# Performance work log

Hardware: AMD Instinct MI355X
Metric: run time of the kernel (lower is better)

## Reference

```python
import jax, jax.numpy as jnp
import numpy as np

N = 5000      # nodes per event (hardcoded in PFNet7.forward)
BIN = 100     # LSH bin_size
K = 16        # kNN per node within bin
SLOPE = 0.01  # LeakyReLU default negative slope


def _mlp(x, W1, b1, W2, b2, W3, b3):
    h = jax.nn.leaky_relu(x @ W1 + b1, SLOPE)
    h = jax.nn.leaky_relu(h @ W2 + b2, SLOPE)
    return h @ W3 + b3


def _build_graph_lsh(x, codebook):
    # x: [N, F]. Faithful vectorized version of GraphBuildingLSH (batch=1).
    n_bins = N // BIN                                   # 50
    mul = x @ codebook[:, : n_bins // 2]                # [N, 25]
    cmul = jnp.concatenate([mul, -mul], axis=-1)        # [N, 50]
    bin_idx = jnp.argmax(cmul, axis=-1)                 # [N]
    bins_split = jnp.argsort(bin_idx).reshape(n_bins, BIN)  # [nb, BIN]
    pts = x[bins_split]                                 # [nb, BIN, F]
    dm = jax.nn.sigmoid(jnp.einsum('pif,pjf->pij', pts, pts))  # [nb, BIN, BIN]
    vals, inds = jax.lax.top_k(dm, K)                   # [nb, BIN, K]
    src = jnp.broadcast_to(bins_split[:, :, None], inds.shape).reshape(-1)
    dst = jnp.take_along_axis(bins_split, inds.reshape(n_bins, -1), axis=1).reshape(-1)
    val = vals.reshape(-1)                              # [nb*BIN*K] = 80000 edges
    return src, dst, val


def _gcn_conv(x, W, b, src, dst, ew):
    # PyG GCNConv: add self-loops (weight 1), symmetric normalization, aggregate at col.
    n = x.shape[0]
    loop = jnp.arange(n)
    row = jnp.concatenate([src, loop])
    col = jnp.concatenate([dst, loop])
    w = jnp.concatenate([ew, jnp.ones((n,), x.dtype)])
    deg = jax.ops.segment_sum(w, col, num_segments=n)
    dis = jnp.where(deg > 0, deg ** -0.5, 0.0)
    norm = dis[row] * w * dis[col]
    h = x @ W
    out = jax.ops.segment_sum(norm[:, None] * h[row], col, num_segments=n)
    return out + b


def _graph_conv(x, Wrel, brel, Wroot, src, dst, ew):
    # PyG GraphConv(aggr='add'): lin_rel(sum_j w_ij x_j) + lin_root(x)
    agg = jax.ops.segment_sum(ew[:, None] * x[src], dst, num_segments=x.shape[0])
    return agg @ Wrel + brel + x @ Wroot


def setup_inputs() -> dict:
    key = jax.random.key(0)
    ks = jax.random.split(key, 24)
    f32 = jnp.float32
    d = {
        'x': jax.random.normal(ks[0], (N, 12), f32),
        'ygen_id': jax.random.normal(ks[1], (N, 6), f32),
        'ygen': jax.random.normal(ks[2], (N, 6), f32),
        'codebook': jax.random.normal(ks[3], (12, 100), f32),
        # nn1: 12 -> 125 -> 125 -> 12
        'nn1_W1': jax.random.normal(ks[4], (12, 125), f32) * 0.1,
        'nn1_b1': jnp.zeros((125,), f32),
        'nn1_W2': jax.random.normal(ks[5], (125, 125), f32) * 0.1,
        'nn1_b2': jnp.zeros((125,), f32),
        'nn1_W3': jax.random.normal(ks[6], (125, 12), f32) * 0.1,
        'nn1_b3': jnp.zeros((12,), f32),
        # GCNConv: 12 -> 32
        'gcn_W': jax.random.normal(ks[7], (12, 32), f32) * 0.1,
        'gcn_b': jnp.zeros((32,), f32),
        # GraphConv: 32 -> 32
        'gc_Wrel': jax.random.normal(ks[8], (32, 32), f32) * 0.1,
        'gc_brel': jnp.zeros((32,), f32),
        'gc_Wroot': jax.random.normal(ks[9], (32, 32), f32) * 0.1,
        # nn2: 32 -> 125 -> 125 -> 6
        'nn2_W1': jax.random.normal(ks[10], (32, 125), f32) * 0.1,
        'nn2_b1': jnp.zeros((125,), f32),
        'nn2_W2': jax.random.normal(ks[11], (125, 125), f32) * 0.1,
        'nn2_b2': jnp.zeros((125,), f32),
        'nn2_W3': jax.random.normal(ks[12], (125, 6), f32) * 0.1,
        'nn2_b3': jnp.zeros((6,), f32),
        # nn3: 38 -> 125 -> 125 -> 6
        'nn3_W1': jax.random.normal(ks[13], (38, 125), f32) * 0.1,
        'nn3_b1': jnp.zeros((125,), f32),
        'nn3_W2': jax.random.normal(ks[14], (125, 125), f32) * 0.1,
        'nn3_b2': jnp.zeros((125,), f32),
        'nn3_W3': jax.random.normal(ks[15], (125, 6), f32) * 0.1,
        'nn3_b3': jnp.zeros((6,), f32),
    }
    return d


def reference(x, ygen_id, ygen, codebook,
              nn1_W1, nn1_b1, nn1_W2, nn1_b2, nn1_W3, nn1_b3,
              gcn_W, gcn_b, gc_Wrel, gc_brel, gc_Wroot,
              nn2_W1, nn2_b1, nn2_W2, nn2_b2, nn2_W3, nn2_b3,
              nn3_W1, nn3_b1, nn3_W2, nn3_b2, nn3_W3, nn3_b3):
    h = _mlp(x, nn1_W1, nn1_b1, nn1_W2, nn1_b2, nn1_W3, nn1_b3)   # [N, 12]
    src, dst, ew = _build_graph_lsh(h, codebook)
    h = jax.nn.leaky_relu(h, SLOPE)
    h = _gcn_conv(h, gcn_W, gcn_b, src, dst, ew)                   # [N, 32]
    h = _graph_conv(h, gc_Wrel, gc_brel, gc_Wroot, src, dst, ew)
    h = jax.nn.leaky_relu(h, SLOPE)
    cand_ids = _mlp(h, nn2_W1, nn2_b1, nn2_W2, nn2_b2, nn2_W3, nn2_b3)
    cand_p4 = _mlp(jnp.concatenate([h, cand_ids], axis=-1),
                   nn3_W1, nn3_b1, nn3_W2, nn3_b2, nn3_W3, nn3_b3)
    return (cand_ids, cand_p4, ygen_id, ygen)
```

## Files before the change

kernel.cpp:

```cpp
#include <hip/hip_runtime.h>
#include <math.h>

#define NN 5000
#define NBINS 50
#define BINSZ 100
#define KNN 16
#define BPAD 104
#define MROWS 112
#define NB 20

typedef _Float16 half8 __attribute__((ext_vector_type(8)));

__device__ __forceinline__ float lrelu(float x){ return x >= 0.f ? x : 0.01f*x; }

__global__ __launch_bounds__(640) void nn1_kernel(
    const float* __restrict__ x,
    const float* __restrict__ W1, const float* __restrict__ b1,
    const float* __restrict__ W2, const float* __restrict__ b2,
    const float* __restrict__ W3, const float* __restrict__ b3,
    const float* __restrict__ cb,
    float* __restrict__ h_out, int* __restrict__ bin_idx) {
    __shared__ float sW[8000];
    __shared__ float bufX[12 * NB];
    __shared__ float bufA[125 * NB];
    __shared__ float bufB[125 * NB];
    __shared__ float sCB[300];
    int tid = threadIdx.x;
    int n0 = blockIdx.x * NB;
    int g = tid >> 7, j = tid & 127;
    float acc[4];
    float4 r0, r1; float rt = 0.f;

    if (tid < 60) {
        float4 v = ((const float4*)(x + n0 * 12))[tid];
        int e = tid * 4;
        bufX[(e % 12) * NB + (e / 12)] = v.x;
        bufX[((e + 1) % 12) * NB + ((e + 1) / 12)] = v.y;
        bufX[((e + 2) % 12) * NB + ((e + 2) / 12)] = v.z;
        bufX[((e + 3) % 12) * NB + ((e + 3) / 12)] = v.w;
    }
    if (tid < 300) { int k = tid / 25, c = tid - k * 25; sCB[tid] = cb[k * 100 + c]; }
    if (tid < 375) ((float4*)sW)[tid] = ((const float4*)W1)[tid];
    __syncthreads();

    if (j < 125) {
        float bj = b1[j];
        acc[0] = bj; acc[1] = bj; acc[2] = bj; acc[3] = bj;
        #pragma unroll
        for (int k = 0; k < 12; ++k) {
            float w = sW[k * 125 + j];
            float4 a = *(const float4*)&bufX[k * NB + g * 4];
            acc[0] += a.x * w; acc[1] += a.y * w; acc[2] += a.z * w; acc[3] += a.w * w;
        }
        #pragma unroll
        for (int n = 0; n < 4; ++n) bufA[j * NB + g * 4 + n] = lrelu(acc[n]);
    }
    r0 = (tid < 1000) ? ((const float4*)W2)[tid] : make_float4(0.f,0.f,0.f,0.f);
    r1 = (tid < 360)  ? ((const float4*)W2)[tid + 640] : make_float4(0.f,0.f,0.f,0.f);
    __syncthreads();
    if (tid < 1000) ((float4*)sW)[tid] = r0;
    if (tid < 360)  ((float4*)sW)[tid + 640] = r1;
    __syncthreads();

    if (j < 125) { float bj = b2[j]; acc[0] = bj; acc[1] = bj; acc[2] = bj; acc[3] = bj; }
    for (int c = 0; c < 4; ++c) {
        if (c < 3) {
            int base = (c + 1) * 1000, nf4 = (c + 1 < 3) ? 1000 : 906;
            r0 = (tid < nf4) ? ((const float4*)W2)[base + tid] : make_float4(0.f,0.f,0.f,0.f);
            r1 = (tid + 640 < nf4) ? ((const float4*)W2)[base + tid + 640] : make_float4(0.f,0.f,0.f,0.f);
            if (c + 1 == 3 && tid == 0) rt = W2[15624];
        }
        int nk = (c < 3) ? 32 : 29;
        const float* wbuf = sW + (c & 1) * 4000;
        if (j < 125) {
            const float* arow = &bufA[(c * 32) * NB + g * 4];
            for (int k = 0; k < nk; ++k) {
                float w = wbuf[k * 125 + j];
                float4 a = *(const float4*)&arow[k * NB];
                acc[0] += a.x * w; acc[1] += a.y * w; acc[2] += a.z * w; acc[3] += a.w * w;
            }
        }
        if (c < 3) {
            float* dst = sW + ((c + 1) & 1) * 4000;
            int nf4 = (c + 1 < 3) ? 1000 : 906;
            if (tid < nf4) ((float4*)dst)[tid] = r0;
            if (tid + 640 < nf4) ((float4*)dst)[tid + 640] = r1;
            if (c + 1 == 3 && tid == 0) dst[3624] = rt;
            __syncthreads();
        }
    }
    if (j < 125) {
        #pragma unroll
        for (int n = 0; n < 4; ++n) bufB[j * NB + g * 4 + n] = lrelu(acc[n]);
    }
    __syncthreads();
    if (tid < 375) ((float4*)sW)[tid] = ((const float4*)W3)[tid];
    __syncthreads();

    if (j < 48) {
        int jj = j % 12, s = j / 12;
        int k0 = s * 32, nk = (s < 3) ? 32 : 29;
        float ps[4] = {0.f, 0.f, 0.f, 0.f};
        for (int k = 0; k < nk; ++k) {
            float w = sW[(k0 + k) * 12 + jj];
            float4 a = *(const float4*)&bufB[(k0 + k) * NB + g * 4];
            ps[0] += a.x * w; ps[1] += a.y * w; ps[2] += a.z * w; ps[3] += a.w * w;
        }
        #pragma unroll
        for (int n = 0; n < 4; ++n) bufA[(s * 12 + jj) * NB + g * 4 + n] = ps[n];
    }
    __syncthreads();
    if (tid < 240) {
        int jj = tid / 20, n = tid % 20;
        float v = bufA[jj * NB + n] + bufA[(12 + jj) * NB + n]
                + bufA[(24 + jj) * NB + n] + bufA[(36 + jj) * NB + n] + b3[jj];
        h_out[(n0 + n) * 12 + jj] = v;
        bufB[jj * NB + n] = v;
    }
    __syncthreads();

    if (tid < NB) {
        int n = tid;
        float hv[12];
        #pragma unroll
        for (int k = 0; k < 12; ++k) hv[k] = bufB[k * NB + n];
        float best = -INFINITY; int bi = 0;
        for (int c = 0; c < 25; ++c) {
            float m = 0.f;
            #pragma unroll
            for (int k = 0; k < 12; ++k) m += hv[k] * sCB[k * 25 + c];
            if (m > best) { best = m; bi = c; }
        }
        for (int c = 0; c < 25; ++c) {
            float m = 0.f;
            #pragma unroll
            for (int k = 0; k < 12; ++k) m += hv[k] * sCB[k * 25 + c];
            if (-m > best) { best = -m; bi = c + 25; }
        }
        bin_idx[n0 + n] = bi;
    }
}

__global__ __launch_bounds__(64) void scatter_kernel(
    const int* __restrict__ bin_idx, int* __restrict__ order) {
    __shared__ int sBI[NN];
    int b = blockIdx.x, lane = threadIdx.x;
    for (int t = lane; t < NN / 4; t += 64) ((int4*)sBI)[t] = ((const int4*)bin_idx)[t];
    __syncthreads();
    unsigned long long below = (lane == 0) ? 0ULL : ((~0ULL) >> (64 - lane));
    int cnt_lt = 0;
    for (int base = 0; base < NN; base += 64) {
        int i = base + lane;
        int bi = (i < NN) ? sBI[i] : 999;
        cnt_lt += __popcll(__ballot(bi < b));
    }
    int offs = cnt_lt;
    for (int base = 0; base < NN; base += 64) {
        int i = base + lane;
        int bi = (i < NN) ? sBI[i] : 999;
        unsigned long long m = __ballot(bi == b);
        if (bi == b) order[offs + __popcll(m & below)] = i;
        offs += __popcll(m);
    }
}

__global__ __launch_bounds__(256) void build_kernel(
    const float* __restrict__ h, const int* __restrict__ order,
    _Float16* __restrict__ Mg, float* __restrict__ dis_g) {
    __shared__ _Float16 M[BINSZ * BPAD];
    __shared__ float s_h[BINSZ * 12];
    __shared__ int   s_nodes[BINSZ];
    __shared__ unsigned s_tv[200 * KNN];
    int p = blockIdx.x, tid = threadIdx.x;

    if (tid < BINSZ) s_nodes[tid] = order[p * BINSZ + tid];
    for (int t = tid; t < BINSZ * BPAD / 2; t += 256) ((int*)M)[t] = 0;
    __syncthreads();
    for (int t = tid; t < BINSZ * 12; t += 256) {
        int i = t / 12, k = t - i * 12;
        s_h[t] = h[s_nodes[i] * 12 + k];
    }
    __syncthreads();

    if (tid < 200) {
        int row = tid >> 1, half = tid & 1;
        const float4* xp = (const float4*)&s_h[row * 12];
        float4 x0 = xp[0], x1 = xp[1], x2 = xp[2];
        unsigned tv[KNN];
        #pragma unroll
        for (int k = 0; k < KNN; ++k) tv[k] = 0u;
        int j0 = half * 50;
        for (int jj = 0; jj < 50; ++jj) {
            int j = j0 + jj;
            const float4* ap = (const float4*)&s_h[j * 12];
            float4 a0 = ap[0], a1 = ap[1], a2 = ap[2];
            float d = x0.x*a0.x + x0.y*a0.y + x0.z*a0.z + x0.w*a0.w
                    + x1.x*a1.x + x1.y*a1.y + x1.z*a1.z + x1.w*a1.w
                    + x2.x*a2.x + x2.y*a2.y + x2.z*a2.z + x2.w*a2.w;
            float v = 1.f / (1.f + expf(-d));
            unsigned key = (__float_as_uint(v) & 0xFFFFFF80u) | (unsigned)(127 - j);
            if (key > tv[KNN - 1]) {
                unsigned ins = key;
                #pragma unroll
                for (int k = 0; k < KNN; ++k) {
                    bool gt = ins > tv[k];
                    unsigned mx = gt ? ins : tv[k];
                    unsigned mn = gt ? tv[k] : ins;
                    tv[k] = mx; ins = mn;
                }
            }
        }
        #pragma unroll
        for (int k = 0; k < KNN; ++k) s_tv[tid * KNN + k] = tv[k];
    }
    __syncthreads();

    if (tid < BINSZ) {
        int base = tid * 32;
        int ia = 0, ib = 0;
        #pragma unroll
        for (int k = 0; k < KNN; ++k) {
            unsigned av = s_tv[base + ia], bv = s_tv[base + 16 + ib];
            bool tA = av > bv;
            unsigned key = tA ? av : bv;
            ia += tA; ib += !tA;
            int ix = 127 - (int)(key & 127u);
            float v = __uint_as_float(key & 0xFFFFFF80u);
            M[ix * BPAD + tid] = (_Float16)v;
        }
    }
    __syncthreads();

    for (int t = tid; t < BINSZ * BPAD / 8; t += 256)
        ((uint4*)(Mg + (size_t)p * BINSZ * BPAD))[t] = ((const uint4*)M)[t];
    if (tid < BINSZ) {
        float dsum = 1.0f;
        #pragma unroll 13
        for (int sc = 0; sc < 13; ++sc) {
            half8 m = *(const half8*)&M[tid * BPAD + sc * 8];
            dsum += (float)m[0] + (float)m[1] + (float)m[2] + (float)m[3]
                  + (float)m[4] + (float)m[5] + (float)m[6] + (float)m[7];
        }
        dis_g[p * BINSZ + tid] = 1.0f / sqrtf(dsum);
    }
}

__global__ __launch_bounds__(128) void conv_kernel(
    const _Float16* __restrict__ Mg, const float* __restrict__ dis_g,
    const float* __restrict__ h, const int* __restrict__ order,
    const float* __restrict__ gcn_W, const float* __restrict__ gcn_b,
    float* __restrict__ gcn_n, float* __restrict__ agg_n,
    const float4* __restrict__ ygen_id4, const float4* __restrict__ ygen4,
    float4* __restrict__ out4) {
    __shared__ _Float16 M[MROWS * BPAD];
    __shared__ float s_h[BINSZ * 12];
    __shared__ int   s_nodes[BINSZ];
    __shared__ float s_dis[BINSZ];
    __shared__ float s_w[12 * 8];
    __shared__ float s_hWd[8 * BPAD];
    __shared__ float s_gcn[8 * BPAD];
    int bid = blockIdx.x, tid = threadIdx.x;
    int p = bid >> 2, cg = bid & 3, c0 = cg * 8;

    if (tid < 75) {
        int gI = bid * 75 + tid;
        out4[15000 + gI] = (gI < 7500) ? ygen_id4[gI] : ygen4[gI - 7500];
    }
    if (tid < BINSZ) {
        s_nodes[tid] = order[p * BINSZ + tid];
        s_dis[tid]   = dis_g[p * BINSZ + tid];
    }
    for (int t = tid; t < 96; t += 128)
        s_w[t] = gcn_W[(t >> 3) * 32 + c0 + (t & 7)];
    for (int t = tid; t < BINSZ * BPAD / 8; t += 128)
        ((uint4*)M)[t] = ((const uint4*)(Mg + (size_t)p * BINSZ * BPAD))[t];
    for (int t = tid; t < (MROWS - BINSZ) * BPAD / 2; t += 128)
        ((int*)(M + BINSZ * BPAD))[t] = 0;
    if (tid < 32) {
        s_hWd[(tid >> 2) * BPAD + 100 + (tid & 3)] = 0.f;
        s_gcn[(tid >> 2) * BPAD + 100 + (tid & 3)] = 0.f;
    }
    __syncthreads();
    for (int t = tid; t < BINSZ * 12; t += 128) {
        int i = t / 12, k = t - i * 12;
        s_h[t] = h[s_nodes[i] * 12 + k];
    }
    __syncthreads();

    for (int o = tid; o < BINSZ * 8; o += 128) {
        int s = o >> 3, cc = o & 7;
        float a = 0.f;
        #pragma unroll
        for (int k = 0; k < 12; ++k) a += lrelu(s_h[s * 12 + k]) * s_w[k * 8 + cc];
        s_hWd[cc * BPAD + s] = s_dis[s] * a;
    }
    __syncthreads();

    int cc = tid & 7, dg = tid >> 3;
    {
        float acc[7];
        #pragma unroll
        for (int r = 0; r < 7; ++r) acc[r] = 0.f;
        for (int sc = 0; sc < 13; ++sc) {
            float4 hv0 = *(const float4*)&s_hWd[cc * BPAD + sc * 8];
            float4 hv1 = *(const float4*)&s_hWd[cc * BPAD + sc * 8 + 4];
            #pragma unroll
            for (int r = 0; r < 7; ++r) {
                int d = dg + 16 * r;
                half8 m = *(const half8*)&M[d * BPAD + sc * 8];
                acc[r] += (float)m[0]*hv0.x + (float)m[1]*hv0.y + (float)m[2]*hv0.z + (float)m[3]*hv0.w
                        + (float)m[4]*hv1.x + (float)m[5]*hv1.y + (float)m[6]*hv1.z + (float)m[7]*hv1.w;
            }
        }
        float bc = gcn_b[c0 + cc];
        #pragma unroll
        for (int r = 0; r < 7; ++r) {
            int d = dg + 16 * r;
            if (d < BINSZ) {
                float gq = s_dis[d] * (acc[r] + s_hWd[cc * BPAD + d]) + bc;
                s_gcn[cc * BPAD + d] = gq;
                gcn_n[s_nodes[d] * 32 + c0 + cc] = gq;
            }
        }
    }
    __syncthreads();
    {
        float acc[7];
        #pragma unroll
        for (int r = 0; r < 7; ++r) acc[r] = 0.f;
        for (int sc = 0; sc < 13; ++sc) {
            float4 hv0 = *(const float4*)&s_gcn[cc * BPAD + sc * 8];
            float4 hv1 = *(const float4*)&s_gcn[cc * BPAD + sc * 8 + 4];
            #pragma unroll
            for (int r = 0; r < 7; ++r) {
                int d = dg + 16 * r;
                half8 m = *(const half8*)&M[d * BPAD + sc * 8];
                acc[r] += (float)m[0]*hv0.x + (float)m[1]*hv0.y + (float)m[2]*hv0.z + (float)m[3]*hv0.w
                        + (float)m[4]*hv1.x + (float)m[5]*hv1.y + (float)m[6]*hv1.z + (float)m[7]*hv1.w;
            }
        }
        #pragma unroll
        for (int r = 0; r < 7; ++r) {
            int d = dg + 16 * r;
            if (d < BINSZ) agg_n[s_nodes[d] * 32 + c0 + cc] = acc[r];
        }
    }
}

__global__ __launch_bounds__(640) void nn23_kernel(
    const float* __restrict__ gcn_n, const float* __restrict__ agg_n,
    const float* __restrict__ Wrel, const float* __restrict__ brel,
    const float* __restrict__ Wroot,
    const float* __restrict__ A1, const float* __restrict__ ab1,
    const float* __restrict__ A2, const float* __restrict__ ab2,
    const float* __restrict__ A3, const float* __restrict__ ab3,
    const float* __restrict__ B1, const float* __restrict__ bb1,
    const float* __restrict__ B2, const float* __restrict__ bb2,
    const float* __restrict__ B3, const float* __restrict__ bb3,
    float* __restrict__ out_ids, float* __restrict__ out_p4) {
    __shared__ float sW[8000];
    __shared__ float sAG[32 * NB];
    __shared__ float sGC[32 * NB];
    __shared__ float bufC[38 * NB];
    __shared__ float bufA[125 * NB];
    __shared__ float bufB[125 * NB];
    int tid = threadIdx.x;
    int n0 = blockIdx.x * NB;
    int g = tid >> 7, j = tid & 127;
    float acc[4];
    float4 r0, r1; float rt = 0.f;

    if (tid < 160) {
        float4 va = ((const float4*)(agg_n + n0 * 32))[tid];
        float4 vg = ((const float4*)(gcn_n + n0 * 32))[tid];
        int e = tid * 4, n = e / 32, k = e % 32;
        sAG[k * NB + n] = va.x; sAG[(k+1) * NB + n] = va.y;
        sAG[(k+2) * NB + n] = va.z; sAG[(k+3) * NB + n] = va.w;
        sGC[k * NB + n] = vg.x; sGC[(k+1) * NB + n] = vg.y;
        sGC[(k+2) * NB + n] = vg.z; sGC[(k+3) * NB + n] = vg.w;
    }
    if (tid >= 160 && tid < 416) ((float4*)sW)[tid - 160] = ((const float4*)Wrel)[tid - 160];
    if (tid >= 416 && tid < 640) ((float4*)(sW + 1024))[tid - 416] = ((const float4*)Wroot)[tid - 416];
    if (tid < 32) ((float4*)(sW + 1024))[224 + tid] = ((const float4*)Wroot)[224 + tid];
    for (int t = tid; t < 1000; t += 640) ((float4*)(sW + 2048))[t] = ((const float4*)A1)[t];
    __syncthreads();

    {
        int jc = tid / 20, n = tid % 20;
        float a = brel[jc];
        #pragma unroll 8
        for (int k = 0; k < 32; ++k)
            a += sAG[k * NB + n] * sW[k * 32 + jc] + sGC[k * NB + n] * sW[1024 + k * 32 + jc];
        bufC[jc * NB + n] = lrelu(a);
    }
    __syncthreads();

    if (j < 125) {
        float bj = ab1[j];
        acc[0] = bj; acc[1] = bj; acc[2] = bj; acc[3] = bj;
        #pragma unroll 8
        for (int k = 0; k < 32; ++k) {
            float w = sW[2048 + k * 125 + j];
            float4 a = *(const float4*)&bufC[k * NB + g * 4];
            acc[0] += a.x * w; acc[1] += a.y * w; acc[2] += a.z * w; acc[3] += a.w * w;
        }
        #pragma unroll
        for (int n = 0; n < 4; ++n) bufA[j * NB + g * 4 + n] = lrelu(acc[n]);
    }
    r0 = (tid < 1000) ? ((const float4*)A2)[tid] : make_float4(0.f,0.f,0.f,0.f);
    r1 = (tid < 360)  ? ((const float4*)A2)[tid + 640] : make_float4(0.f,0.f,0.f,0.f);
    __syncthreads();
    if (tid < 1000) ((float4*)sW)[tid] = r0;
    if (tid < 360)  ((float4*)sW)[tid + 640] = r1;
    __syncthreads();

    if (j < 125) { float bj = ab2[j]; acc[0] = bj; acc[1] = bj; acc[2] = bj; acc[3] = bj; }
    for (int c = 0; c < 4; ++c) {
        if (c < 3) {
            int base = (c + 1) * 1000, nf4 = (c + 1 < 3) ? 1000 : 906;
            r0 = (tid < nf4) ? ((const float4*)A2)[base + tid] : make_float4(0.f,0.f,0.f,0.f);
            r1 = (tid + 640 < nf4) ? ((const float4*)A2)[base + tid + 640] : make_float4(0.f,0.f,0.f,0.f);
            if (c + 1 == 3 && tid == 0) rt = A2[15624];
        }
        int nk = (c < 3) ? 32 : 29;
        const float* wbuf = sW + (c & 1) * 4000;
        if (j < 125) {
            const float* arow = &bufA[(c * 32) * NB + g * 4];
            for (int k = 0; k < nk; ++k) {
                float w = wbuf[k * 125 + j];
                float4 a = *(const float4*)&arow[k * NB];
                acc[0] += a.x * w; acc[1] += a.y * w; acc[2] += a.z * w; acc[3] += a.w * w;
            }
        }
        if (c < 3) {
            float* dst = sW + ((c + 1) & 1) * 4000;
            int nf4 = (c + 1 < 3) ? 1000 : 906;
            if (tid < nf4) ((float4*)dst)[tid] = r0;
            if (tid + 640 < nf4) ((float4*)dst)[tid + 640] = r1;
            if (c + 1 == 3 && tid == 0) dst[3624] = rt;
            __syncthreads();
        }
    }
    if (j < 125) {
        #pragma unroll
        for (int n = 0; n < 4; ++n) bufB[j * NB + g * 4 + n] = lrelu(acc[n]);
    }
    __syncthreads();
    if (tid < 187) ((float4*)sW)[tid] = ((const float4*)A3)[tid];
    if (tid == 187) { sW[748] = A3[748]; sW[749] = A3[749]; }
    for (int t = tid; t < 1187; t += 640) ((float4*)(sW + 752))[t] = ((const float4*)B1)[t];
    if (tid == 188) { sW[752 + 4748] = B1[4748]; sW[752 + 4749] = B1[4749]; }
    __syncthreads();

    if (j < 24) {
        int jj = j % 6, s = j / 6;
        int k0 = s * 32, nk = (s < 3) ? 32 : 29;
        float ps[4] = {0.f, 0.f, 0.f, 0.f};
        for (int k = 0; k < nk; ++k) {
            float w = sW[(k0 + k) * 6 + jj];
            float4 a = *(const float4*)&bufB[(k0 + k) * NB + g * 4];
            ps[0] += a.x * w; ps[1] += a.y * w; ps[2] += a.z * w; ps[3] += a.w * w;
        }
        #pragma unroll
        for (int n = 0; n < 4; ++n) bufA[(s * 6 + jj) * NB + g * 4 + n] = ps[n];
    }
    __syncthreads();
    if (tid < 120) {
        int jj = tid / 20, n = tid % 20;
        float v = bufA[jj * NB + n] + bufA[(6 + jj) * NB + n]
                + bufA[(12 + jj) * NB + n] + bufA[(18 + jj) * NB + n] + ab3[jj];
        out_ids[(n0 + n) * 6 + jj] = v;
        bufC[(32 + jj) * NB + n] = v;
    }
    __syncthreads();

    if (j < 125) {
        float bj = bb1[j];
        acc[0] = bj; acc[1] = bj; acc[2] = bj; acc[3] = bj;
        #pragma unroll 2
        for (int k = 0; k < 38; ++k) {
            float w = sW[752 + k * 125 + j];
            float4 a = *(const float4*)&bufC[k * NB + g * 4];
            acc[0] += a.x * w; acc[1] += a.y * w; acc[2] += a.z * w; acc[3] += a.w * w;
        }
        #pragma unroll
        for (int n = 0; n < 4; ++n) bufA[j * NB + g * 4 + n] = lrelu(acc[n]);
    }
    r0 = (tid < 1000) ? ((const float4*)B2)[tid] : make_float4(0.f,0.f,0.f,0.f);
    r1 = (tid < 360)  ? ((const float4*)B2)[tid + 640] : make_float4(0.f,0.f,0.f,0.f);
    __syncthreads();
    if (tid < 1000) ((float4*)sW)[tid] = r0;
    if (tid < 360)  ((float4*)sW)[tid + 640] = r1;
    __syncthreads();

    if (j < 125) { float bj = bb2[j]; acc[0] = bj; acc[1] = bj; acc[2] = bj; acc[3] = bj; }
    for (int c = 0; c < 4; ++c) {
        if (c < 3) {
            int base = (c + 1) * 1000, nf4 = (c + 1 < 3) ? 1000 : 906;
            r0 = (tid < nf4) ? ((const float4*)B2)[base + tid] : make_float4(0.f,0.f,0.f,0.f);
            r1 = (tid + 640 < nf4) ? ((const float4*)B2)[base + tid + 640] : make_float4(0.f,0.f,0.f,0.f);
            if (c + 1 == 3 && tid == 0) rt = B2[15624];
        }
        int nk = (c < 3) ? 32 : 29;
        const float* wbuf = sW + (c & 1) * 4000;
        if (j < 125) {
            const float* arow = &bufA[(c * 32) * NB + g * 4];
            for (int k = 0; k < nk; ++k) {
                float w = wbuf[k * 125 + j];
                float4 a = *(const float4*)&arow[k * NB];
                acc[0] += a.x * w; acc[1] += a.y * w; acc[2] += a.z * w; acc[3] += a.w * w;
            }
        }
        if (c < 3) {
            float* dst = sW + ((c + 1) & 1) * 4000;
            int nf4 = (c + 1 < 3) ? 1000 : 906;
            if (tid < nf4) ((float4*)dst)[tid] = r0;
            if (tid + 640 < nf4) ((float4*)dst)[tid + 640] = r1;
            if (c + 1 == 3 && tid == 0) dst[3624] = rt;
            __syncthreads();
        }
    }
    if (j < 125) {
        #pragma unroll
        for (int n = 0; n < 4; ++n) bufB[j * NB + g * 4 + n] = lrelu(acc[n]);
    }
    __syncthreads();
    if (tid < 187) ((float4*)sW)[tid] = ((const float4*)B3)[tid];
    if (tid == 187) { sW[748] = B3[748]; sW[749] = B3[749]; }
    __syncthreads();

    if (j < 24) {
        int jj = j % 6, s = j / 6;
        int k0 = s * 32, nk = (s < 3) ? 32 : 29;
        float ps[4] = {0.f, 0.f, 0.f, 0.f};
        for (int k = 0; k < nk; ++k) {
            float w = sW[(k0 + k) * 6 + jj];
            float4 a = *(const float4*)&bufB[(k0 + k) * NB + g * 4];
            ps[0] += a.x * w; ps[1] += a.y * w; ps[2] += a.z * w; ps[3] += a.w * w;
        }
        #pragma unroll
        for (int n = 0; n < 4; ++n) bufA[(s * 6 + jj) * NB + g * 4 + n] = ps[n];
    }
    __syncthreads();
    if (tid < 120) {
        int jj = tid / 20, n = tid % 20;
        float v = bufA[jj * NB + n] + bufA[(6 + jj) * NB + n]
                + bufA[(12 + jj) * NB + n] + bufA[(18 + jj) * NB + n] + bb3[jj];
        out_p4[(n0 + n) * 6 + jj] = v;
    }
}

static inline int cdiv(int a, int b) { return (a + b - 1) / b; }

extern "C" void kernel_launch(void* const* d_in, const int* in_sizes, int n_in,
                              void* d_out, int out_size, void* d_ws, size_t ws_size,
                              hipStream_t stream) {
    const float* x        = (const float*)d_in[0];
    const float* ygen_id  = (const float*)d_in[1];
    const float* ygen     = (const float*)d_in[2];
    const float* codebook = (const float*)d_in[3];
    const float* nn1_W1 = (const float*)d_in[4];  const float* nn1_b1 = (const float*)d_in[5];
    const float* nn1_W2 = (const float*)d_in[6];  const float* nn1_b2 = (const float*)d_in[7];
    const float* nn1_W3 = (const float*)d_in[8];  const float* nn1_b3 = (const float*)d_in[9];
    const float* gcn_W  = (const float*)d_in[10]; const float* gcn_b  = (const float*)d_in[11];
    const float* gc_Wrel = (const float*)d_in[12]; const float* gc_brel = (const float*)d_in[13];
    const float* gc_Wroot = (const float*)d_in[14];
    const float* nn2_W1 = (const float*)d_in[15]; const float* nn2_b1 = (const float*)d_in[16];
    const float* nn2_W2 = (const float*)d_in[17]; const float* nn2_b2 = (const float*)d_in[18];
    const float* nn2_W3 = (const float*)d_in[19]; const float* nn2_b3 = (const float*)d_in[20];
    const float* nn3_W1 = (const float*)d_in[21]; const float* nn3_b1 = (const float*)d_in[22];
    const float* nn3_W2 = (const float*)d_in[23]; const float* nn3_b2 = (const float*)d_in[24];
    const float* nn3_W3 = (const float*)d_in[25]; const float* nn3_b3 = (const float*)d_in[26];

    float* out = (float*)d_out;
    float* ws  = (float*)d_ws;

    float* h      = ws + 0;
    float* gcn_n  = ws + 60000;
    float* agg_n  = ws + 220000;
    float* dis_g  = ws + 380000;
    _Float16* Mg  = (_Float16*)(ws + 385000);
    int* bin_idx  = (int*)(ws + 645000);
    int* order    = (int*)(ws + 650000);

    nn1_kernel<<<NN / NB, 640, 0, stream>>>(
        x, nn1_W1, nn1_b1, nn1_W2, nn1_b2, nn1_W3, nn1_b3, codebook,
        h, bin_idx);

    scatter_kernel<<<NBINS, 64, 0, stream>>>(bin_idx, order);

    build_kernel<<<NBINS, 256, 0, stream>>>(h, order, Mg, dis_g);

    conv_kernel<<<NBINS * 4, 128, 0, stream>>>(
        Mg, dis_g, h, order, gcn_W, gcn_b, gcn_n, agg_n,
        (const float4*)ygen_id, (const float4*)ygen, (float4*)out);

    nn23_kernel<<<NN / NB, 640, 0, stream>>>(
        gcn_n, agg_n, gc_Wrel, gc_brel, gc_Wroot,
        nn2_W1, nn2_b1, nn2_W2, nn2_b2, nn2_W3, nn2_b3,
        nn3_W1, nn3_b1, nn3_W2, nn3_b2, nn3_W3, nn3_b3,
        out, out + 30000);
}
```

Before: 196.4 us.

## Fuse graph build with GCN conv and register-tile the 125x125 MLP layers

Merges build_kernel and conv_kernel into one 640-thread kernel per bin. The adjacency matrix and degree normalization now stay in shared memory instead of making a round trip through global memory, and one kernel launch disappears. Separately, the 125x125 hidden layers in nn1 and nn23 store weights padded to a 128-float row stride, and each thread computes a 4x2 output tile using float4 weight loads, which raises arithmetic per shared-memory load. The trade-off is that the fused kernel runs only 50 blocks instead of 200, which lowers parallelism for the conv stage, and the weight scatter into shared memory uses scalar stores.

```diff
diff --git a/kernel.cpp b/kernel.cpp
--- a/kernel.cpp
+++ b/kernel.cpp
@@ -6,12 +6,19 @@
 #define BINSZ 100
 #define KNN 16
 #define BPAD 104
-#define MROWS 112
 #define NB 20
 
 typedef _Float16 half8 __attribute__((ext_vector_type(8)));
 
 __device__ __forceinline__ float lrelu(float x){ return x >= 0.f ? x : 0.01f*x; }
+
+__device__ __forceinline__ void scatter_w(float* dst, int t, float4 v) {
+    int e = 4 * t, r = e / 125, c = e - 125 * r;
+    dst[r * 128 + c] = v.x; if (++c == 125) { c = 0; ++r; }
+    dst[r * 128 + c] = v.y; if (++c == 125) { c = 0; ++r; }
+    dst[r * 128 + c] = v.z; if (++c == 125) { c = 0; ++r; }
+    dst[r * 128 + c] = v.w;
+}
 
 __global__ __launch_bounds__(640) void nn1_kernel(
     const float* __restrict__ x,
@@ -20,7 +27,7 @@
     const float* __restrict__ W3, const float* __restrict__ b3,
     const float* __restrict__ cb,
     float* __restrict__ h_out, int* __restrict__ bin_idx) {
-    __shared__ float sW[8000];
+    __shared__ float sW[8192];
     __shared__ float bufX[12 * NB];
     __shared__ float bufA[125 * NB];
     __shared__ float bufB[125 * NB];
@@ -58,11 +65,20 @@
     r0 = (tid < 1000) ? ((const float4*)W2)[tid] : make_float4(0.f,0.f,0.f,0.f);
     r1 = (tid < 360)  ? ((const float4*)W2)[tid + 640] : make_float4(0.f,0.f,0.f,0.f);
     __syncthreads();
-    if (tid < 1000) ((float4*)sW)[tid] = r0;
-    if (tid < 360)  ((float4*)sW)[tid + 640] = r1;
-    __syncthreads();
-
-    if (j < 125) { float bj = b2[j]; acc[0] = bj; acc[1] = bj; acc[2] = bj; acc[3] = bj; }
+    if (tid < 1000) scatter_w(sW, tid, r0);
+    if (tid < 360)  scatter_w(sW, tid + 640, r1);
+    __syncthreads();
+
+    float acc8[8];
+    if (tid < 320) {
+        int j4 = tid & 31;
+        #pragma unroll
+        for (int jj = 0; jj < 4; ++jj) {
+            int jc = 4 * j4 + jj;
+            float bj = (jc < 125) ? b2[jc] : 0.f;
+            acc8[2 * jj] = bj; acc8[2 * jj + 1] = bj;
+        }
+    }
     for (int c = 0; c < 4; ++c) {
         if (c < 3) {
             int base = (c + 1) * 1000, nf4 = (c + 1 < 3) ? 1000 : 906;
@@ -71,27 +87,38 @@
             if (c + 1 == 3 && tid == 0) rt = W2[15624];
         }
         int nk = (c < 3) ? 32 : 29;
-        const float* wbuf = sW + (c & 1) * 4000;
-        if (j < 125) {
-            const float* arow = &bufA[(c * 32) * NB + g * 4];
+        if (tid < 320) {
+            int j4 = tid & 31, n2 = tid >> 5;
+            const float* wbuf = sW + (c & 1) * 4096;
+            const float* arow = bufA + (c * 32) * NB + 2 * n2;
             for (int k = 0; k < nk; ++k) {
-                float w = wbuf[k * 125 + j];
-                float4 a = *(const float4*)&arow[k * NB];
-                acc[0] += a.x * w; acc[1] += a.y * w; acc[2] += a.z * w; acc[3] += a.w * w;
+                float4 w4 = *(const float4*)&wbuf[k * 128 + 4 * j4];
+                float2 a2 = *(const float2*)&arow[k * NB];
+                acc8[0] += w4.x * a2.x; acc8[1] += w4.x * a2.y;
+                acc8[2] += w4.y * a2.x; acc8[3] += w4.y * a2.y;
+                acc8[4] += w4.z * a2.x; acc8[5] += w4.z * a2.y;
+                acc8[6] += w4.w * a2.x; acc8[7] += w4.w * a2.y;
             }
         }
         if (c < 3) {
-            float* dst = sW + ((c + 1) & 1) * 4000;
+            float* dst = sW + ((c + 1) & 1) * 4096;
             int nf4 = (c + 1 < 3) ? 1000 : 906;
-            if (tid < nf4) ((float4*)dst)[tid] = r0;
-            if (tid + 640 < nf4) ((float4*)dst)[tid + 640] = r1;
-            if (c + 1 == 3 && tid == 0) dst[3624] = rt;
+            if (tid < nf4) scatter_w(dst, tid, r0);
+            if (tid + 640 < nf4) scatter_w(dst, tid + 640, r1);
+            if (c + 1 == 3 && tid == 0) dst[3708] = rt;
             __syncthreads();
         }
     }
-    if (j < 125) {
-        #pragma unroll
-        for (int n = 0; n < 4; ++n) bufB[j * NB + g * 4 + n] = lrelu(acc[n]);
+    if (tid < 320) {
+        int j4 = tid & 31, n2 = tid >> 5;
+        #pragma unroll
+        for (int jj = 0; jj < 4; ++jj) {
+            int jc = 4 * j4 + jj;
+            if (jc < 125) {
+                bufB[jc * NB + 2 * n2]     = lrelu(acc8[2 * jj]);
+                bufB[jc * NB + 2 * n2 + 1] = lrelu(acc8[2 * jj + 1]);
+            }
+        }
     }
     __syncthreads();
     if (tid < 375) ((float4*)sW)[tid] = ((const float4*)W3)[tid];
@@ -164,19 +191,32 @@
     }
 }
 
-__global__ __launch_bounds__(256) void build_kernel(
+__global__ __launch_bounds__(640) void graph2_kernel(
     const float* __restrict__ h, const int* __restrict__ order,
-    _Float16* __restrict__ Mg, float* __restrict__ dis_g) {
+    const float* __restrict__ gcn_W, const float* __restrict__ gcn_b,
+    float* __restrict__ gcn_n, float* __restrict__ agg_n,
+    const float4* __restrict__ ygen_id4, const float4* __restrict__ ygen4,
+    float4* __restrict__ out4) {
     __shared__ _Float16 M[BINSZ * BPAD];
     __shared__ float s_h[BINSZ * 12];
     __shared__ int   s_nodes[BINSZ];
-    __shared__ unsigned s_tv[200 * KNN];
+    __shared__ float s_dis[BINSZ];
+    __shared__ float s_w[12 * 32];
+    __shared__ float s_big[2 * 32 * BPAD];
+    float* s_hWd = s_big;
+    float* s_gcn = s_big + 32 * BPAD;
+    unsigned* s_tv = (unsigned*)s_big;
     int p = blockIdx.x, tid = threadIdx.x;
 
     if (tid < BINSZ) s_nodes[tid] = order[p * BINSZ + tid];
-    for (int t = tid; t < BINSZ * BPAD / 2; t += 256) ((int*)M)[t] = 0;
-    __syncthreads();
-    for (int t = tid; t < BINSZ * 12; t += 256) {
+    for (int t = tid; t < BINSZ * BPAD / 2; t += 640) ((int*)M)[t] = 0;
+    if (tid < 384) s_w[tid] = gcn_W[tid];
+    if (tid < 300) {
+        int gI = p * 300 + tid;
+        out4[15000 + gI] = (gI < 7500) ? ygen_id4[gI] : ygen4[gI - 7500];
+    }
+    __syncthreads();
+    for (int t = tid; t < BINSZ * 12; t += 640) {
         int i = t / 12, k = t - i * 12;
         s_h[t] = h[s_nodes[i] * 12 + k];
     }
@@ -231,8 +271,6 @@
     }
     __syncthreads();
 
-    for (int t = tid; t < BINSZ * BPAD / 8; t += 256)
-        ((uint4*)(Mg + (size_t)p * BINSZ * BPAD))[t] = ((const uint4*)M)[t];
     if (tid < BINSZ) {
         float dsum = 1.0f;
         #pragma unroll 13
@@ -241,108 +279,64 @@
             dsum += (float)m[0] + (float)m[1] + (float)m[2] + (float)m[3]
                   + (float)m[4] + (float)m[5] + (float)m[6] + (float)m[7];
         }
-        dis_g[p * BINSZ + tid] = 1.0f / sqrtf(dsum);
-    }
-}
-
-__global__ __launch_bounds__(128) void conv_kernel(
-    const _Float16* __restrict__ Mg, const float* __restrict__ dis_g,
-    const float* __restrict__ h, const int* __restrict__ order,
-    const float* __restrict__ gcn_W, const float* __restrict__ gcn_b,
-    float* __restrict__ gcn_n, float* __restrict__ agg_n,
-    const float4* __restrict__ ygen_id4, const float4* __restrict__ ygen4,
-    float4* __restrict__ out4) {
-    __shared__ _Float16 M[MROWS * BPAD];
-    __shared__ float s_h[BINSZ * 12];
-    __shared__ int   s_nodes[BINSZ];
-    __shared__ float s_dis[BINSZ];
-    __shared__ float s_w[12 * 8];
-    __shared__ float s_hWd[8 * BPAD];
-    __shared__ float s_gcn[8 * BPAD];
-    int bid = blockIdx.x, tid = threadIdx.x;
-    int p = bid >> 2, cg = bid & 3, c0 = cg * 8;
-
-    if (tid < 75) {
-        int gI = bid * 75 + tid;
-        out4[15000 + gI] = (gI < 7500) ? ygen_id4[gI] : ygen4[gI - 7500];
-    }
-    if (tid < BINSZ) {
-        s_nodes[tid] = order[p * BINSZ + tid];
-        s_dis[tid]   = dis_g[p * BINSZ + tid];
-    }
-    for (int t = tid; t < 96; t += 128)
-        s_w[t] = gcn_W[(t >> 3) * 32 + c0 + (t & 7)];
-    for (int t = tid; t < BINSZ * BPAD / 8; t += 128)
-        ((uint4*)M)[t] = ((const uint4*)(Mg + (size_t)p * BINSZ * BPAD))[t];
-    for (int t = tid; t < (MROWS - BINSZ) * BPAD / 2; t += 128)
-        ((int*)(M + BINSZ * BPAD))[t] = 0;
-    if (tid < 32) {
+        s_dis[tid] = 1.0f / sqrtf(dsum);
+    }
+    __syncthreads();
+
+    for (int o = tid; o < BINSZ * 32; o += 640) {
+        int s = o >> 5, cc = o & 31;
+        float a = 0.f;
+        #pragma unroll
+        for (int k = 0; k < 12; ++k) a += lrelu(s_h[s * 12 + k]) * s_w[k * 32 + cc];
+        s_hWd[cc * BPAD + s] = s_dis[s] * a;
+    }
+    if (tid < 128) {
         s_hWd[(tid >> 2) * BPAD + 100 + (tid & 3)] = 0.f;
         s_gcn[(tid >> 2) * BPAD + 100 + (tid & 3)] = 0.f;
     }
     __syncthreads();
-    for (int t = tid; t < BINSZ * 12; t += 128) {
-        int i = t / 12, k = t - i * 12;
-        s_h[t] = h[s_nodes[i] * 12 + k];
-    }
-    __syncthreads();
-
-    for (int o = tid; o < BINSZ * 8; o += 128) {
-        int s = o >> 3, cc = o & 7;
-        float a = 0.f;
-        #pragma unroll
-        for (int k = 0; k < 12; ++k) a += lrelu(s_h[s * 12 + k]) * s_w[k * 8 + cc];
-        s_hWd[cc * BPAD + s] = s_dis[s] * a;
-    }
-    __syncthreads();
-
-    int cc = tid & 7, dg = tid >> 3;
+
+    int cc = tid & 31, dgg = tid >> 5;
     {
-        float acc[7];
-        #pragma unroll
-        for (int r = 0; r < 7; ++r) acc[r] = 0.f;
+        float a5[5] = {0.f, 0.f, 0.f, 0.f, 0.f};
         for (int sc = 0; sc < 13; ++sc) {
             float4 hv0 = *(const float4*)&s_hWd[cc * BPAD + sc * 8];
             float4 hv1 = *(const float4*)&s_hWd[cc * BPAD + sc * 8 + 4];
             #pragma unroll
-            for (int r = 0; r < 7; ++r) {
-                int d = dg + 16 * r;
+            for (int r = 0; r < 5; ++r) {
+                int d = dgg + 20 * r;
                 half8 m = *(const half8*)&M[d * BPAD + sc * 8];
-                acc[r] += (float)m[0]*hv0.x + (float)m[1]*hv0.y + (float)m[2]*hv0.z + (float)m[3]*hv0.w
-                        + (float)m[4]*hv1.x + (float)m[5]*hv1.y + (float)m[6]*hv1.z + (float)m[7]*hv1.w;
-            }
-        }
-        float bc = gcn_b[c0 + cc];
-        #pragma unroll
-        for (int r = 0; r < 7; ++r) {
-            int d = dg + 16 * r;
-            if (d < BINSZ) {
-                float gq = s_dis[d] * (acc[r] + s_hWd[cc * BPAD + d]) + bc;
-                s_gcn[cc * BPAD + d] = gq;
-                gcn_n[s_nodes[d] * 32 + c0 + cc] = gq;
-            }
+                a5[r] += (float)m[0]*hv0.x + (float)m[1]*hv0.y + (float)m[2]*hv0.z + (float)m[3]*hv0.w
+                       + (float)m[4]*hv1.x + (float)m[5]*hv1.y + (float)m[6]*hv1.z + (float)m[7]*hv1.w;
+            }
+        }
+        float bc = gcn_b[cc];
+        #pragma unroll
+        for (int r = 0; r < 5; ++r) {
+            int d = dgg + 20 * r;
+            float gq = s_dis[d] * (a5[r] + s_hWd[cc * BPAD + d]) + bc;
+            s_gcn[cc * BPAD + d] = gq;
+            gcn_n[s_nodes[d] * 32 + cc] = gq;
         }
     }
     __syncthreads();
     {
-        float acc[7];
-        #pragma unroll
-        for (int r = 0; r < 7; ++r) acc[r] = 0.f;
+        float a5[5] = {0.f, 0.f, 0.f, 0.f, 0.f};
         for (int sc = 0; sc < 13; ++sc) {
             float4 hv0 = *(const float4*)&s_gcn[cc * BPAD + sc * 8];
             float4 hv1 = *(const float4*)&s_gcn[cc * BPAD + sc * 8 + 4];
             #pragma unroll
-            for (int r = 0; r < 7; ++r) {
-                int d = dg + 16 * r;
+            for (int r = 0; r < 5; ++r) {
+                int d = dgg + 20 * r;
                 half8 m = *(const half8*)&M[d * BPAD + sc * 8];
-                acc[r] += (float)m[0]*hv0.x + (float)m[1]*hv0.y + (float)m[2]*hv0.z + (float)m[3]*hv0.w
-                        + (float)m[4]*hv1.x + (float)m[5]*hv1.y + (float)m[6]*hv1.z + (float)m[7]*hv1.w;
-            }
-        }
-        #pragma unroll
-        for (int r = 0; r < 7; ++r) {
-            int d = dg + 16 * r;
-            if (d < BINSZ) agg_n[s_nodes[d] * 32 + c0 + cc] = acc[r];
+                a5[r] += (float)m[0]*hv0.x + (float)m[1]*hv0.y + (float)m[2]*hv0.z + (float)m[3]*hv0.w
+                       + (float)m[4]*hv1.x + (float)m[5]*hv1.y + (float)m[6]*hv1.z + (float)m[7]*hv1.w;
+            }
+        }
+        #pragma unroll
+        for (int r = 0; r < 5; ++r) {
+            int d = dgg + 20 * r;
+            agg_n[s_nodes[d] * 32 + cc] = a5[r];
         }
     }
 }
@@ -358,7 +352,7 @@
     const float* __restrict__ B2, const float* __restrict__ bb2,
     const float* __restrict__ B3, const float* __restrict__ bb3,
     float* __restrict__ out_ids, float* __restrict__ out_p4) {
-    __shared__ float sW[8000];
+    __shared__ float sW[8192];
     __shared__ float sAG[32 * NB];
     __shared__ float sGC[32 * NB];
     __shared__ float bufC[38 * NB];
@@ -368,6 +362,7 @@
     int n0 = blockIdx.x * NB;
     int g = tid >> 7, j = tid & 127;
     float acc[4];
+    float acc8[8];
     float4 r0, r1; float rt = 0.f;
 
     if (tid < 160) {
@@ -410,11 +405,19 @@
     r0 = (tid < 1000) ? ((const float4*)A2)[tid] : make_float4(0.f,0.f,0.f,0.f);
     r1 = (tid < 360)  ? ((const float4*)A2)[tid + 640] : make_float4(0.f,0.f,0.f,0.f);
     __syncthreads();
-    if (tid < 1000) ((float4*)sW)[tid] = r0;
-    if (tid < 360)  ((float4*)sW)[tid + 640] = r1;
-    __syncthreads();
-
-    if (j < 125) { float bj = ab2[j]; acc[0] = bj; acc[1] = bj; acc[2] = bj; acc[3] = bj; }
+    if (tid < 1000) scatter_w(sW, tid, r0);
+    if (tid < 360)  scatter_w(sW, tid + 640, r1);
+    __syncthreads();
+
+    if (tid < 320) {
+        int j4 = tid & 31;
+        #pragma unroll
+        for (int jj = 0; jj < 4; ++jj) {
+            int jc = 4 * j4 + jj;
+            float bj = (jc < 125) ? ab2[jc] : 0.f;
+            acc8[2 * jj] = bj; acc8[2 * jj + 1] = bj;
+        }
+    }
     for (int c = 0; c < 4; ++c) {
         if (c < 3) {
             int base = (c + 1) * 1000, nf4 = (c + 1 < 3) ? 1000 : 906;
@@ -423,27 +426,38 @@
             if (c + 1 == 3 && tid == 0) rt = A2[15624];
         }
         int nk = (c < 3) ? 32 : 29;
-        const float* wbuf = sW + (c & 1) * 4000;
-        if (j < 125) {
-            const float* arow = &bufA[(c * 32) * NB + g * 4];
+        if (tid < 320) {
+            int j4 = tid & 31, n2 = tid >> 5;
+            const float* wbuf = sW + (c & 1) * 4096;
+            const float* arow = bufA + (c * 32) * NB + 2 * n2;
             for (int k = 0; k < nk; ++k) {
-                float w = wbuf[k * 125 + j];
-                float4 a = *(const float4*)&arow[k * NB];
-                acc[0] += a.x * w; acc[1] += a.y * w; acc[2] += a.z * w; acc[3] += a.w * w;
+                float4 w4 = *(const float4*)&wbuf[k * 128 + 4 * j4];
+                float2 a2 = *(const float2*)&arow[k * NB];
+                acc8[0] += w4.x * a2.x; acc8[1] += w4.x * a2.y;
+                acc8[2] += w4.y * a2.x; acc8[3] += w4.y * a2.y;
+                acc8[4] += w4.z * a2.x; acc8[5] += w4.z * a2.y;
+                acc8[6] += w4.w * a2.x; acc8[7] += w4.w * a2.y;
             }
         }
         if (c < 3) {
-            float* dst = sW + ((c + 1) & 1) * 4000;
+            float* dst = sW + ((c + 1) & 1) * 4096;
             int nf4 = (c + 1 < 3) ? 1000 : 906;
-            if (tid < nf4) ((float4*)dst)[tid] = r0;
-            if (tid + 640 < nf4) ((float4*)dst)[tid + 640] = r1;
-            if (c + 1 == 3 && tid == 0) dst[3624] = rt;
+            if (tid < nf4) scatter_w(dst, tid, r0);
+            if (tid + 640 < nf4) scatter_w(dst, tid + 640, r1);
+            if (c + 1 == 3 && tid == 0) dst[3708] = rt;
             __syncthreads();
         }
     }
-    if (j < 125) {
-        #pragma unroll
-        for (int n = 0; n < 4; ++n) bufB[j * NB + g * 4 + n] = lrelu(acc[n]);
+    if (tid < 320) {
+        int j4 = tid & 31, n2 = tid >> 5;
+        #pragma unroll
+        for (int jj = 0; jj < 4; ++jj) {
+            int jc = 4 * j4 + jj;
+            if (jc < 125) {
+                bufB[jc * NB + 2 * n2]     = lrelu(acc8[2 * jj]);
+                bufB[jc * NB + 2 * n2 + 1] = lrelu(acc8[2 * jj + 1]);
+            }
+        }
     }
     __syncthreads();
     if (tid < 187) ((float4*)sW)[tid] = ((const float4*)A3)[tid];
@@ -489,11 +503,19 @@
     r0 = (tid < 1000) ? ((const float4*)B2)[tid] : make_float4(0.f,0.f,0.f,0.f);
     r1 = (tid < 360)  ? ((const float4*)B2)[tid + 640] : make_float4(0.f,0.f,0.f,0.f);
     __syncthreads();
-    if (tid < 1000) ((float4*)sW)[tid] = r0;
-    if (tid < 360)  ((float4*)sW)[tid + 640] = r1;
-    __syncthreads();
-
-    if (j < 125) { float bj = bb2[j]; acc[0] = bj; acc[1] = bj; acc[2] = bj; acc[3] = bj; }
+    if (tid < 1000) scatter_w(sW, tid, r0);
+    if (tid < 360)  scatter_w(sW, tid + 640, r1);
+    __syncthreads();
+
+    if (tid < 320) {
+        int j4 = tid & 31;
+        #pragma unroll
+        for (int jj = 0; jj < 4; ++jj) {
+            int jc = 4 * j4 + jj;
+            float bj = (jc < 125) ? bb2[jc] : 0.f;
+            acc8[2 * jj] = bj; acc8[2 * jj + 1] = bj;
+        }
+    }
     for (int c = 0; c < 4; ++c) {
         if (c < 3) {
             int base = (c + 1) * 1000, nf4 = (c + 1 < 3) ? 1000 : 906;
@@ -502,27 +524,38 @@
             if (c + 1 == 3 && tid == 0) rt = B2[15624];
         }
         int nk = (c < 3) ? 32 : 29;
-        const float* wbuf = sW + (c & 1) * 4000;
-        if (j < 125) {
-            const float* arow = &bufA[(c * 32) * NB + g * 4];
+        if (tid < 320) {
+            int j4 = tid & 31, n2 = tid >> 5;
+            const float* wbuf = sW + (c & 1) * 4096;
+            const float* arow = bufA + (c * 32) * NB + 2 * n2;
             for (int k = 0; k < nk; ++k) {
-                float w = wbuf[k * 125 + j];
-                float4 a = *(const float4*)&arow[k * NB];
-                acc[0] += a.x * w; acc[1] += a.y * w; acc[2] += a.z * w; acc[3] += a.w * w;
+                float4 w4 = *(const float4*)&wbuf[k * 128 + 4 * j4];
+                float2 a2 = *(const float2*)&arow[k * NB];
+                acc8[0] += w4.x * a2.x; acc8[1] += w4.x * a2.y;
+                acc8[2] += w4.y * a2.x; acc8[3] += w4.y * a2.y;
+                acc8[4] += w4.z * a2.x; acc8[5] += w4.z * a2.y;
+                acc8[6] += w4.w * a2.x; acc8[7] += w4.w * a2.y;
             }
         }
         if (c < 3) {
-            float* dst = sW + ((c + 1) & 1) * 4000;
+            float* dst = sW + ((c + 1) & 1) * 4096;
             int nf4 = (c + 1 < 3) ? 1000 : 906;
-            if (tid < nf4) ((float4*)dst)[tid] = r0;
-            if (tid + 640 < nf4) ((float4*)dst)[tid + 640] = r1;
-            if (c + 1 == 3 && tid == 0) dst[3624] = rt;
+            if (tid < nf4) scatter_w(dst, tid, r0);
+            if (tid + 640 < nf4) scatter_w(dst, tid + 640, r1);
+            if (c + 1 == 3 && tid == 0) dst[3708] = rt;
             __syncthreads();
         }
     }
-    if (j < 125) {
-        #pragma unroll
-        for (int n = 0; n < 4; ++n) bufB[j * NB + g * 4 + n] = lrelu(acc[n]);
+    if (tid < 320) {
+        int j4 = tid & 31, n2 = tid >> 5;
+        #pragma unroll
+        for (int jj = 0; jj < 4; ++jj) {
+            int jc = 4 * j4 + jj;
+            if (jc < 125) {
+                bufB[jc * NB + 2 * n2]     = lrelu(acc8[2 * jj]);
+                bufB[jc * NB + 2 * n2 + 1] = lrelu(acc8[2 * jj + 1]);
+            }
+        }
     }
     __syncthreads();
     if (tid < 187) ((float4*)sW)[tid] = ((const float4*)B3)[tid];
@@ -578,10 +611,8 @@
     float* h      = ws + 0;
     float* gcn_n  = ws + 60000;
     float* agg_n  = ws + 220000;
-    float* dis_g  = ws + 380000;
-    _Float16* Mg  = (_Float16*)(ws + 385000);
-    int* bin_idx  = (int*)(ws + 645000);
-    int* order    = (int*)(ws + 650000);
+    int* bin_idx  = (int*)(ws + 380000);
+    int* order    = (int*)(ws + 385000);
 
     nn1_kernel<<<NN / NB, 640, 0, stream>>>(
         x, nn1_W1, nn1_b1, nn1_W2, nn1_b2, nn1_W3, nn1_b3, codebook,
@@ -589,10 +620,8 @@
 
     scatter_kernel<<<NBINS, 64, 0, stream>>>(bin_idx, order);
 
-    build_kernel<<<NBINS, 256, 0, stream>>>(h, order, Mg, dis_g);
-
-    conv_kernel<<<NBINS * 4, 128, 0, stream>>>(
-        Mg, dis_g, h, order, gcn_W, gcn_b, gcn_n, agg_n,
+    graph2_kernel<<<NBINS, 640, 0, stream>>>(
+        h, order, gcn_W, gcn_b, gcn_n, agg_n,
         (const float4*)ygen_id, (const float4*)ygen, (float4*)out);
 
     nn23_kernel<<<NN / NB, 640, 0, stream>>>(
```

Result: no change. 199.6 us (+1.6%).
